# Performance work log

Hardware: AMD Instinct MI355X
Metric: run time of the kernel (lower is better)

## Reference

```python
import jax, jax.numpy as jnp
import numpy as np

B, S, DIN, DOUT = 2, 2048, 4096, 4096


def setup_inputs() -> dict:
    key = jax.random.key(0)
    k1, k2 = jax.random.split(key)
    x = jax.random.normal(k1, (B, S, DIN), dtype=jnp.float32)
    weight = jax.random.normal(k2, (DOUT, DIN), dtype=jnp.float32) * 0.02
    # xnor init for row scaling pattern
    mean = weight.mean(-1, keepdims=True)                      # [DOUT,1]
    scale = jnp.abs(weight - mean).mean(-1, keepdims=True)     # [DOUT,1]
    wscale = scale
    wbias = mean
    return {"x": x, "weight": weight, "wscale": wscale, "wbias": wbias}


def reference(x, weight, wscale, wbias):
    # STE binarization: forward = sign(weight) (grad handled in bwd module)
    w_bin = jnp.sign(weight)
    w = wscale * w_bin + wbias                                 # [DOUT, DIN]
    # F.linear(x, w): x @ w.T, no bias
    out = jnp.einsum('bsk,nk->bsn', x, w)
    return out
```

## Files before the change

kernel.cpp:

```cpp
#include <hip/hip_runtime.h>
#include <stdint.h>


#define MDIM 4096
#define NDIM 4096
#define KDIM 4096

typedef int int4v __attribute__((ext_vector_type(4)));

__device__ __forceinline__ int pack4_rn(float a, float b, float c, float d, float inv) {
  int ia = __float2int_rn(a * inv) & 0xff;
  int ib = __float2int_rn(b * inv) & 0xff;
  int ic = __float2int_rn(c * inv) & 0xff;
  int id = __float2int_rn(d * inv) & 0xff;
  return ia | (ib << 8) | (ic << 16) | (id << 24);
}

__device__ __forceinline__ int sgn8(float v) {
  return (v > 0.f) ? 1 : ((v < 0.f) ? 0xff : 0);
}

#define PREP_XB 1024
#define PREP_WB 1024
__global__ __launch_bounds__(256) void prep_kernel(
    const float* __restrict__ x, const float* __restrict__ w,
    char* __restrict__ xq, char* __restrict__ wsg,
    float* __restrict__ xscale, float* __restrict__ sumx) {
  const int b = blockIdx.x;
  const int tid = threadIdx.x;
  const int lane = tid & 63, wv = tid >> 6;
  if (b < PREP_XB) {
    const int row = b * 4 + wv;
    const float4* xr = (const float4*)(x + (size_t)row * KDIM);
    float4 v[16];
    float s = 0.f, amax = 0.f;
#pragma unroll
    for (int u = 0; u < 16; ++u) {
      v[u] = xr[u * 64 + lane];
      s += v[u].x + v[u].y + v[u].z + v[u].w;
      amax = fmaxf(amax, fmaxf(fmaxf(fabsf(v[u].x), fabsf(v[u].y)),
                               fmaxf(fabsf(v[u].z), fabsf(v[u].w))));
    }
#pragma unroll
    for (int off = 32; off > 0; off >>= 1) {
      s += __shfl_xor(s, off, 64);
      amax = fmaxf(amax, __shfl_xor(amax, off, 64));
    }
    if (lane == 0) {
      sumx[row] = s;
      xscale[row] = amax * (1.f / 127.f);
    }
    const float inv = (amax > 0.f) ? 127.f / amax : 0.f;
    int* xo = (int*)(xq + (size_t)row * KDIM);
#pragma unroll
    for (int u = 0; u < 16; ++u)
      xo[u * 64 + lane] = pack4_rn(v[u].x, v[u].y, v[u].z, v[u].w, inv);
  } else {
    const float4* wr = (const float4*)w;
    int* wo = (int*)wsg;
    const size_t i0 = (size_t)(b - PREP_XB) * 256 + tid;
    const size_t stride = (size_t)PREP_WB * 256;
#pragma unroll
    for (int u = 0; u < 16; ++u) {
      size_t i = i0 + (size_t)u * stride;
      float4 vv = wr[i];
      wo[i] = sgn8(vv.x) | (sgn8(vv.y) << 8) | (sgn8(vv.z) << 16) | (sgn8(vv.w) << 24);
    }
  }
}

__global__ __launch_bounds__(512, 2) void gemm_bin_i8_r128(
    const char* __restrict__ A, const char* __restrict__ Bs,
    const float* __restrict__ wscale, const float* __restrict__ wbias,
    const float* __restrict__ xscale, const float* __restrict__ sumx,
    float* __restrict__ C) {
  __shared__ __align__(16) char sm[131072];

  const int bid = blockIdx.x;
  const int xcd = bid & 7, loc = bid >> 3;
  const int bm = (xcd >> 1) * 4 + (loc >> 3);
  const int bn = (xcd & 1) * 8 + (loc & 7);
  const int tm0 = bm * 256, tn0 = bn * 256;
  const int tid = threadIdx.x;
  const int lane = tid & 63, wave = tid >> 6;
  const int l15 = lane & 15, q4 = lane >> 4, l7 = lane & 7;
  const int wr = wave >> 2, wc = wave & 3;

  int4v acc[8][4];
#pragma unroll
  for (int fr = 0; fr < 8; ++fr)
#pragma unroll
    for (int fc = 0; fc < 4; ++fc) acc[fr][fc] = (int4v){0, 0, 0, 0};

  int4v af[4], bq[4];

  int aAddr[2], bAddr[2];
#pragma unroll
  for (int kh = 0; kh < 2; ++kh) {
    aAddr[kh] = (wr * 128 + l15) * 128 + (((kh * 4 + q4) ^ l7) & 7) * 16;
    bAddr[kh] = 65536 + (wc * 64 + l15) * 128 + (((kh * 4 + q4) ^ l7) & 7) * 16;
  }

  const int u0 = tid, u1 = tid + 512;
  const int gOff0 = (u0 >> 3) * KDIM + (((u0 & 7) ^ ((u0 >> 3) & 7))) * 16;
  const int gOff1 = (u1 >> 3) * KDIM + (((u1 & 7) ^ ((u1 >> 3) & 7))) * 16;
  const int ld0 = tid * 16, ld1 = 8192 + tid * 16;
  const char* Ab = A + (size_t)tm0 * KDIM;
  const char* Bb = Bs + (size_t)tn0 * KDIM;

#define STAGE_A(BUF, RHALF, KOFS)                                                 \
  do {                                                                            \
    const char* g_ = Ab + (RHALF) * 128 * KDIM + (KOFS);                          \
    const int d_ = (BUF) * 32768 + (RHALF) * 16384;                               \
    __builtin_amdgcn_global_load_lds(                                             \
        (const __attribute__((address_space(1))) void*)(g_ + gOff0),              \
        (__attribute__((address_space(3))) void*)(sm + d_ + ld0), 16, 0, 0);      \
    __builtin_amdgcn_global_load_lds(                                             \
        (const __attribute__((address_space(1))) void*)(g_ + gOff1),              \
        (__attribute__((address_space(3))) void*)(sm + d_ + ld1), 16, 0, 0);      \
  } while (0)

#define STAGE_B(BUF, RHALF, KOFS)                                                 \
  do {                                                                            \
    const char* g_ = Bb + (RHALF) * 128 * KDIM + (KOFS);                          \
    const int d_ = 65536 + (BUF) * 32768 + (RHALF) * 16384;                       \
    __builtin_amdgcn_global_load_lds(                                             \
        (const __attribute__((address_space(1))) void*)(g_ + gOff0),              \
        (__attribute__((address_space(3))) void*)(sm + d_ + ld0), 16, 0, 0);      \
    __builtin_amdgcn_global_load_lds(                                             \
        (const __attribute__((address_space(1))) void*)(g_ + gOff1),              \
        (__attribute__((address_space(3))) void*)(sm + d_ + ld1), 16, 0, 0);      \
  } while (0)

#define BARO __builtin_amdgcn_s_barrier()
#define LG0                                                                       \
  do {                                                                            \
    asm volatile("s_waitcnt lgkmcnt(0)" ::: "memory");                            \
    __builtin_amdgcn_sched_barrier(0);                                            \
  } while (0)
#define CKV0 asm volatile("s_waitcnt vmcnt(0)\n\ts_barrier" ::: "memory")

#define PH(BUF, KH, RH, LOADB, STAGEOP, ENDSYNC)                                  \
  do {                                                                            \
    _Pragma("unroll") for (int i_ = 0; i_ < 4; ++i_)                              \
        af[i_] = *(const int4v*)(sm + (BUF) * 32768 + aAddr[KH] +                 \
                                 ((RH) * 4 + i_) * 2048);                         \
    if (LOADB) {                                                                  \
      _Pragma("unroll") for (int j_ = 0; j_ < 4; ++j_)                            \
          bq[j_] = *(const int4v*)(sm + (BUF) * 32768 + bAddr[KH] + j_ * 2048);   \
    }                                                                             \
    STAGEOP;                                                                      \
    BARO;                                                                         \
    LG0;                                                                          \
    __builtin_amdgcn_s_setprio(1);                                                \
    _Pragma("unroll") for (int i_ = 0; i_ < 4; ++i_)                              \
        _Pragma("unroll") for (int j_ = 0; j_ < 4; ++j_)                          \
            acc[(RH) * 4 + i_][j_] = __builtin_amdgcn_mfma_i32_16x16x64_i8(       \
                af[i_], bq[j_], acc[(RH) * 4 + i_][j_], 0, 0, 0);                 \
    __builtin_amdgcn_s_setprio(0);                                                \
    ENDSYNC;                                                                      \
  } while (0)

#define TILE(BUF, TAU)                                                            \
  do {                                                                            \
    PH(BUF, 0, 0, 1, STAGE_A((BUF) ^ 1, 0, ((TAU) + 1) * 128), BARO);             \
    PH(BUF, 0, 1, 0, STAGE_A((BUF) ^ 1, 1, ((TAU) + 1) * 128), BARO);             \
    PH(BUF, 1, 0, 1, STAGE_B((BUF) ^ 1, 0, ((TAU) + 1) * 128), BARO);             \
    PH(BUF, 1, 1, 0, STAGE_B((BUF) ^ 1, 1, ((TAU) + 1) * 128), CKV0);             \
  } while (0)

  STAGE_A(0, 0, 0);
  STAGE_A(0, 1, 0);
  STAGE_B(0, 0, 0);
  STAGE_B(0, 1, 0);
  CKV0;

#pragma unroll 1
  for (int t = 0; t < 30; t += 2) {
    TILE(0, t);
    TILE(1, t + 1);
  }
  TILE(0, 30);
  PH(1, 0, 0, 1, (void)0, BARO);
  PH(1, 0, 1, 0, (void)0, BARO);
  PH(1, 1, 0, 1, (void)0, BARO);
  PH(1, 1, 1, 0, (void)0, (void)0);

#undef TILE
#undef PH
#undef BARO
#undef LG0
#undef CKV0
#undef STAGE_A
#undef STAGE_B

  float wsv[4], wbv[4];
#pragma unroll
  for (int fc = 0; fc < 4; ++fc) {
    int n = tn0 + wc * 64 + fc * 16 + l15;
    wsv[fc] = wscale[n];
    wbv[fc] = wbias[n];
  }
#pragma unroll
  for (int fr = 0; fr < 8; ++fr) {
#pragma unroll
    for (int reg = 0; reg < 4; ++reg) {
      int m = tm0 + wr * 128 + fr * 16 + q4 * 4 + reg;
      float xs = xscale[m];
      float sx = sumx[m];
      float* crow = C + (size_t)m * NDIM + tn0 + wc * 64 + l15;
#pragma unroll
      for (int fc = 0; fc < 4; ++fc)
        crow[fc * 16] = wsv[fc] * xs * (float)acc[fr][fc][reg] + wbv[fc] * sx;
    }
  }
}

extern "C" void kernel_launch(void* const* d_in, const int* in_sizes, int n_in,
                              void* d_out, int out_size, void* d_ws, size_t ws_size,
                              hipStream_t stream) {
  const float* x      = (const float*)d_in[0];
  const float* weight = (const float*)d_in[1];
  const float* wscale = (const float*)d_in[2];
  const float* wbias  = (const float*)d_in[3];
  float* out = (float*)d_out;

  char* xq  = (char*)d_ws;
  char* wsg = xq + (size_t)MDIM * KDIM;
  float* xscale = (float*)(wsg + (size_t)NDIM * KDIM);
  float* sumx   = xscale + MDIM;

  prep_kernel<<<PREP_XB + PREP_WB, 256, 0, stream>>>(
      x, weight, xq, wsg, xscale, sumx);
  gemm_bin_i8_r128<<<(MDIM / 256) * (NDIM / 256), 512, 0, stream>>>(
      xq, wsg, wscale, wbias, xscale, sumx, out);
}
```

Measured before the change: 232.0 us.

## Double-buffer LDS fragment registers so reads overlap MFMA in int8 GEMM

Splits the A and B register fragments into two alternating sets, so the LDS reads for the next phase are issued before the MFMAs of the current phase. Partial lgkmcnt waits replace the full drain. All eight global-to-LDS loads for the next K tile are now issued in one batch at the start of each tile instead of being spread across phases. This hides LDS read latency behind matrix math, at the cost of more registers and a burstier global load pattern.

```diff
diff --git a/kernel.cpp b/kernel.cpp
--- a/kernel.cpp
+++ b/kernel.cpp
@@ -69,7 +69,7 @@
   }
 }
 
-__global__ __launch_bounds__(512, 2) void gemm_bin_i8_r128(
+__global__ __launch_bounds__(512, 2) void gemm_bin_i8_ra128(
     const char* __restrict__ A, const char* __restrict__ Bs,
     const float* __restrict__ wscale, const float* __restrict__ wbias,
     const float* __restrict__ xscale, const float* __restrict__ sumx,
@@ -92,7 +92,7 @@
 #pragma unroll
     for (int fc = 0; fc < 4; ++fc) acc[fr][fc] = (int4v){0, 0, 0, 0};
 
-  int4v af[4], bq[4];
+  int4v afX[4], afY[4], bq0[4], bq1[4];
 
   int aAddr[2], bAddr[2];
 #pragma unroll
@@ -108,72 +108,71 @@
   const char* Ab = A + (size_t)tm0 * KDIM;
   const char* Bb = Bs + (size_t)tn0 * KDIM;
 
-#define STAGE_A(BUF, RHALF, KOFS)                                                 \
-  do {                                                                            \
-    const char* g_ = Ab + (RHALF) * 128 * KDIM + (KOFS);                          \
-    const int d_ = (BUF) * 32768 + (RHALF) * 16384;                               \
-    __builtin_amdgcn_global_load_lds(                                             \
-        (const __attribute__((address_space(1))) void*)(g_ + gOff0),              \
-        (__attribute__((address_space(3))) void*)(sm + d_ + ld0), 16, 0, 0);      \
-    __builtin_amdgcn_global_load_lds(                                             \
-        (const __attribute__((address_space(1))) void*)(g_ + gOff1),              \
-        (__attribute__((address_space(3))) void*)(sm + d_ + ld1), 16, 0, 0);      \
-  } while (0)
-
-#define STAGE_B(BUF, RHALF, KOFS)                                                 \
-  do {                                                                            \
-    const char* g_ = Bb + (RHALF) * 128 * KDIM + (KOFS);                          \
-    const int d_ = 65536 + (BUF) * 32768 + (RHALF) * 16384;                       \
-    __builtin_amdgcn_global_load_lds(                                             \
-        (const __attribute__((address_space(1))) void*)(g_ + gOff0),              \
-        (__attribute__((address_space(3))) void*)(sm + d_ + ld0), 16, 0, 0);      \
-    __builtin_amdgcn_global_load_lds(                                             \
-        (const __attribute__((address_space(1))) void*)(g_ + gOff1),              \
-        (__attribute__((address_space(3))) void*)(sm + d_ + ld1), 16, 0, 0);      \
-  } while (0)
-
-#define BARO __builtin_amdgcn_s_barrier()
-#define LG0                                                                       \
-  do {                                                                            \
-    asm volatile("s_waitcnt lgkmcnt(0)" ::: "memory");                            \
-    __builtin_amdgcn_sched_barrier(0);                                            \
-  } while (0)
-#define CKV0 asm volatile("s_waitcnt vmcnt(0)\n\ts_barrier" ::: "memory")
-
-#define PH(BUF, KH, RH, LOADB, STAGEOP, ENDSYNC)                                  \
+#define GLL(GP, DP)                                                               \
+  __builtin_amdgcn_global_load_lds(                                               \
+      (const __attribute__((address_space(1))) void*)(GP),                        \
+      (__attribute__((address_space(3))) void*)(DP), 16, 0, 0)
+
+#define STAGE8(BUF, KOFS)                                                         \
+  do {                                                                            \
+    const int da_ = (BUF) * 32768;                                                \
+    const int db_ = 65536 + (BUF) * 32768;                                        \
+    GLL(Ab + gOff0 + (KOFS), sm + da_ + ld0);                                     \
+    GLL(Ab + gOff1 + (KOFS), sm + da_ + ld1);                                     \
+    GLL(Ab + 128 * KDIM + gOff0 + (KOFS), sm + da_ + 16384 + ld0);                \
+    GLL(Ab + 128 * KDIM + gOff1 + (KOFS), sm + da_ + 16384 + ld1);                \
+    GLL(Bb + gOff0 + (KOFS), sm + db_ + ld0);                                     \
+    GLL(Bb + gOff1 + (KOFS), sm + db_ + ld1);                                     \
+    GLL(Bb + 128 * KDIM + gOff0 + (KOFS), sm + db_ + 16384 + ld0);                \
+    GLL(Bb + 128 * KDIM + gOff1 + (KOFS), sm + db_ + 16384 + ld1);                \
+  } while (0)
+
+#define DSA(SET, BUF, KH, RH)                                                     \
   do {                                                                            \
     _Pragma("unroll") for (int i_ = 0; i_ < 4; ++i_)                              \
-        af[i_] = *(const int4v*)(sm + (BUF) * 32768 + aAddr[KH] +                 \
-                                 ((RH) * 4 + i_) * 2048);                         \
-    if (LOADB) {                                                                  \
-      _Pragma("unroll") for (int j_ = 0; j_ < 4; ++j_)                            \
-          bq[j_] = *(const int4v*)(sm + (BUF) * 32768 + bAddr[KH] + j_ * 2048);   \
-    }                                                                             \
-    STAGEOP;                                                                      \
-    BARO;                                                                         \
-    LG0;                                                                          \
-    __builtin_amdgcn_s_setprio(1);                                                \
+        af##SET[i_] = *(const int4v*)(sm + (BUF) * 32768 + aAddr[KH] +            \
+                                      ((RH) * 4 + i_) * 2048);                    \
+  } while (0)
+
+#define DSB(SET, BUF, KH)                                                         \
+  do {                                                                            \
+    _Pragma("unroll") for (int j_ = 0; j_ < 4; ++j_)                              \
+        bq##SET[j_] = *(const int4v*)(sm + (BUF) * 32768 + bAddr[KH] + j_ * 2048);\
+  } while (0)
+
+#define MM(ASET, QSET, RH)                                                        \
+  do {                                                                            \
     _Pragma("unroll") for (int i_ = 0; i_ < 4; ++i_)                              \
         _Pragma("unroll") for (int j_ = 0; j_ < 4; ++j_)                          \
             acc[(RH) * 4 + i_][j_] = __builtin_amdgcn_mfma_i32_16x16x64_i8(       \
-                af[i_], bq[j_], acc[(RH) * 4 + i_][j_], 0, 0, 0);                 \
-    __builtin_amdgcn_s_setprio(0);                                                \
-    ENDSYNC;                                                                      \
-  } while (0)
-
-#define TILE(BUF, TAU)                                                            \
-  do {                                                                            \
-    PH(BUF, 0, 0, 1, STAGE_A((BUF) ^ 1, 0, ((TAU) + 1) * 128), BARO);             \
-    PH(BUF, 0, 1, 0, STAGE_A((BUF) ^ 1, 1, ((TAU) + 1) * 128), BARO);             \
-    PH(BUF, 1, 0, 1, STAGE_B((BUF) ^ 1, 0, ((TAU) + 1) * 128), BARO);             \
-    PH(BUF, 1, 1, 0, STAGE_B((BUF) ^ 1, 1, ((TAU) + 1) * 128), CKV0);             \
-  } while (0)
-
-  STAGE_A(0, 0, 0);
-  STAGE_A(0, 1, 0);
-  STAGE_B(0, 0, 0);
-  STAGE_B(0, 1, 0);
+                af##ASET[i_], bq##QSET[j_], acc[(RH) * 4 + i_][j_], 0, 0, 0);     \
+  } while (0)
+
+#define WAITL(N)                                                                  \
+  do {                                                                            \
+    asm volatile("s_waitcnt lgkmcnt(" #N ")" ::: "memory");                       \
+    __builtin_amdgcn_sched_barrier(0);                                            \
+  } while (0)
+#define BARO __builtin_amdgcn_s_barrier()
+#define CKV0 asm volatile("s_waitcnt vmcnt(0)\n\ts_barrier" ::: "memory")
+
+#define TILE(B, TAU)                                                              \
+  do {                                                                            \
+     DSA(Y, B, 0, 1);                                                     \
+    STAGE8((B) ^ 1, ((TAU) + 1) * 128);                                           \
+    WAITL(4); MM(X, 0, 0); BARO;                                                  \
+     DSA(X, B, 1, 0); DSB(1, B, 1);                                       \
+    WAITL(8); MM(Y, 0, 1); BARO;                                                  \
+     DSA(Y, B, 1, 1);                                                     \
+    WAITL(4); MM(X, 1, 0); CKV0;                                                  \
+     DSA(X, (B) ^ 1, 0, 0); DSB(0, (B) ^ 1, 0);                           \
+    WAITL(8); MM(Y, 1, 1); BARO;                                                  \
+  } while (0)
+
+  STAGE8(0, 0);
   CKV0;
+  DSA(X, 0, 0, 0);
+  DSB(0, 0, 0);
 
 #pragma unroll 1
   for (int t = 0; t < 30; t += 2) {
@@ -181,18 +180,23 @@
     TILE(1, t + 1);
   }
   TILE(0, 30);
-  PH(1, 0, 0, 1, (void)0, BARO);
-  PH(1, 0, 1, 0, (void)0, BARO);
-  PH(1, 1, 0, 1, (void)0, BARO);
-  PH(1, 1, 1, 0, (void)0, (void)0);
+  DSA(Y, 1, 0, 1);
+  WAITL(4); MM(X, 0, 0); BARO;
+  DSA(X, 1, 1, 0); DSB(1, 1, 1);
+  WAITL(8); MM(Y, 0, 1); BARO;
+  DSA(Y, 1, 1, 1);
+  WAITL(4); MM(X, 1, 0); BARO;
+  WAITL(0); MM(Y, 1, 1);
 
 #undef TILE
-#undef PH
+#undef CKV0
 #undef BARO
-#undef LG0
-#undef CKV0
-#undef STAGE_A
-#undef STAGE_B
+#undef WAITL
+#undef MM
+#undef DSB
+#undef DSA
+#undef STAGE8
+#undef GLL
 
   float wsv[4], wbv[4];
 #pragma unroll
@@ -232,6 +236,6 @@
 
   prep_kernel<<<PREP_XB + PREP_WB, 256, 0, stream>>>(
       x, weight, xq, wsg, xscale, sumx);
-  gemm_bin_i8_r128<<<(MDIM / 256) * (NDIM / 256), 512, 0, stream>>>(
+  gemm_bin_i8_ra128<<<(MDIM / 256) * (NDIM / 256), 512, 0, stream>>>(
       xq, wsg, wscale, wbias, xscale, sumx, out);
 }
```

Result: no change. 228.5 us (-1.5%).
